# Performance work log

Measured on AMD Instinct MI355X. Metric: run time of the kernel, lower is better.

The kernel has to match this reference:

```python
import jax, jax.numpy as jnp
import numpy as np

SR = 44100.0
BLK = 512          # block_size (hop)
WL = 2048          # win_length
W4 = WL // 4
B, NF = 4, 512
L = NF * BLK


def _framewise_conv(src, kernels, pad_l, pad_r):
    """Per-(batch,frame) 1D cross-correlation via grouped conv.
    src: (B,F,blk), kernels: (B,F,kw) -> (B,F,blk+pad_l+pad_r-kw+1)."""
    b, f, blk = src.shape
    kw = kernels.shape[-1]
    s = jnp.pad(src, ((0, 0), (0, 0), (pad_l, pad_r))).reshape(1, b * f, blk + pad_l + pad_r)
    k = kernels.reshape(b * f, 1, kw)
    out = jax.lax.conv_general_dilated(
        s, k, window_strides=(1,), padding='VALID',
        feature_group_count=b * f, dimension_numbers=('NCH', 'OIH', 'NCH'))
    return out.reshape(b, f, -1)


def _overlap_add(frames, hop, out_len):
    """frames: (B,F,FL) -> (B,out_len) overlap-add with stride hop (== F.fold)."""
    b, f, fl = frames.shape
    idx = jnp.arange(f)[:, None] * hop + jnp.arange(fl)[None, :]  # (F,FL)
    out = jnp.zeros((b, out_len), frames.dtype)
    return out.at[:, idx].add(frames)


def setup_inputs() -> dict:
    key = jax.random.key(0)
    k1, k2, k3, k4, k5 = jax.random.split(key, 5)
    f0_frames = jax.random.uniform(k1, (B, NF, 1), jnp.float32) * 320.0 + 80.0  # 80-400 Hz
    hk = jax.random.normal(k2, (B, NF, WL), jnp.float32) * (1.0 / np.sqrt(WL))
    hks = jax.random.normal(k3, (B, NF, W4), jnp.float32) * (1.0 / np.sqrt(W4))
    nk = jax.random.normal(k4, (B, NF, W4), jnp.float32) * (1.0 / np.sqrt(W4))
    static_noise = jax.random.uniform(k5, (WL * 127,), jnp.float32) * 2.0 - 1.0
    return {"f0_frames": f0_frames, "harmonic_filt_kernel": hk,
            "harmonic_filt_kernel_short": hks, "noise_filt_kernel": nk,
            "static_noise": static_noise}


def reference(f0_frames, harmonic_filt_kernel, harmonic_filt_kernel_short,
              noise_filt_kernel, static_noise):
    b, nf, _ = f0_frames.shape
    # f0 upsampled to sample rate: (B, L)
    f0 = jnp.repeat(f0_frames, BLK, axis=2).reshape(b, -1)
    # phase accumulator, fractional part (f0 > 0 so frac == mod 1)
    x = jnp.mod(jnp.cumsum(f0 / SR, axis=1), 1.0)
    pix = jnp.pi * x
    a = jnp.round(SR / jnp.clip(f0, 20.0, None) * 0.5) * 2.0 + 1.0
    # band-limited impulse-train-like harmonic source (Dirichlet kernel)
    harmonic_source = jnp.where(pix < 1e-8, 1.0,
                                jnp.sin(a * pix) / (a * jnp.sin(pix)))
    harmonic_source = harmonic_source.reshape(b, nf, BLK)
    # tiled static noise, same for all batch items
    reps = L // static_noise.shape[0] + 1
    noise = jnp.tile(static_noise * 0.3162, reps)[:L].reshape(1, nf, BLK)
    noise = jnp.broadcast_to(noise, (b, nf, BLK))
    # short per-frame FIR on harmonic source and noise (kernel len WL//4)
    hs_short = _framewise_conv(harmonic_source, harmonic_filt_kernel_short, W4, W4 - 1)
    nz = _framewise_conv(noise, noise_filt_kernel, W4, W4 - 1)
    # overlap-add mix, crop to L samples
    mix = _overlap_add(nz + hs_short, BLK, L + W4)[:, :L]
    # long per-frame FIR (kernel len WL) on the mixed signal
    src2 = mix.reshape(b, nf, BLK)
    h2 = _framewise_conv(src2, harmonic_filt_kernel, WL, WL - 1)
    out = _overlap_add(h2, BLK, L + WL)[:, :L]
    return jnp.clip(out, -1.0, 1.0)
```

## Files before the change

kernel.cpp:

```cpp
#include <hip/hip_runtime.h>


#define BLKS  512
#define WL    2048
#define W4    512
#define NB    4
#define NFR   512
#define LTOT  (NFR*BLKS)
#define NCH   (LTOT/16)
#define SN_LEN 260096

typedef float f4 __attribute__((ext_vector_type(4)));

static __device__ __forceinline__ void seg4(const float* __restrict__ P, int c0,
                                            const float* __restrict__ S,
                                            float&a0,float&a1,float&a2,float&a3) {
    f4 A = *(const f4*)(P + c0 - 4);
    #pragma unroll 4
    for (int m0 = 0; m0 < 512; m0 += 4) {
        f4 B = *(const f4*)(P + c0 + m0);
        f4 x = *(const f4*)(S + m0);
        a0 += B.x*x.x; a0 += B.y*x.y; a0 += B.z*x.z; a0 += B.w*x.w;
        a1 += A.w*x.x; a1 += B.x*x.y; a1 += B.y*x.z; a1 += B.z*x.w;
        a2 += A.z*x.x; a2 += A.w*x.y; a2 += B.x*x.z; a2 += B.y*x.w;
        a3 += A.y*x.x; a3 += A.z*x.y; a3 += A.w*x.z; a3 += B.x*x.w;
        A = B;
    }
}

static __device__ __forceinline__ void segmix(const float* __restrict__ Ph,
                                              const float* __restrict__ Pn, int c0,
                                              const float* __restrict__ Sh,
                                              const float* __restrict__ Sn,
                                              float&a0,float&a1,float&a2,float&a3) {
    f4 Ah = *(const f4*)(Ph + c0 - 4);
    f4 An = *(const f4*)(Pn + c0 - 4);
    #pragma unroll 4
    for (int m0 = 0; m0 < 512; m0 += 4) {
        f4 Bh = *(const f4*)(Ph + c0 + m0);
        f4 Bn = *(const f4*)(Pn + c0 + m0);
        f4 xh = *(const f4*)(Sh + m0);
        f4 xr = *(const f4*)(Sn + m0);
        f4 xn; xn.x = xr.x*0.3162f; xn.y = xr.y*0.3162f;
               xn.z = xr.z*0.3162f; xn.w = xr.w*0.3162f;
        a0 += Bh.x*xh.x; a0 += Bn.x*xn.x;  a0 += Bh.y*xh.y; a0 += Bn.y*xn.y;
        a0 += Bh.z*xh.z; a0 += Bn.z*xn.z;  a0 += Bh.w*xh.w; a0 += Bn.w*xn.w;
        a1 += Ah.w*xh.x; a1 += An.w*xn.x;  a1 += Bh.x*xh.y; a1 += Bn.x*xn.y;
        a1 += Bh.y*xh.z; a1 += Bn.y*xn.z;  a1 += Bh.z*xh.w; a1 += Bn.z*xn.w;
        a2 += Ah.z*xh.x; a2 += An.z*xn.x;  a2 += Ah.w*xh.y; a2 += An.w*xn.y;
        a2 += Bh.x*xh.z; a2 += Bn.x*xn.z;  a2 += Bh.y*xh.w; a2 += Bn.y*xn.w;
        a3 += Ah.y*xh.x; a3 += An.y*xn.x;  a3 += Ah.z*xh.y; a3 += An.z*xn.y;
        a3 += Ah.w*xh.z; a3 += An.w*xn.z;  a3 += Bh.x*xh.w; a3 += Bn.x*xn.w;
        Ah = Bh; An = Bn;
    }
}

__global__ void __launch_bounds__(256) k_scan_a(const float* __restrict__ f0_frames,
                                                float* __restrict__ L0,
                                                float* __restrict__ L1) {
    int b = blockIdx.y;
    int chunk = blockIdx.x * 256 + threadIdx.x;
    int g0 = chunk * 16;
    float d = f0_frames[b*NFR + (g0 >> 9)] / 44100.0f;
    float* o = L0 + (size_t)b*LTOT + g0;
    float acc = 0.0f;
    #pragma unroll
    for (int j = 0; j < 16; ++j) { acc = acc + d; o[j] = acc; }
    L1[(size_t)b*NCH + chunk] = acc;
}

__global__ void __launch_bounds__(1024) k_scan_b(float* __restrict__ L1g) {
    __shared__ float sL2[1024];
    __shared__ float sL3[64];
    __shared__ float sL4[4];
    int b = blockIdx.x, tid = threadIdx.x;
    float* L1 = L1g + (size_t)b*NCH;
    {
        float* p = L1 + tid*16;
        float acc = 0.0f;
        #pragma unroll
        for (int j = 0; j < 16; ++j) { acc = acc + p[j]; p[j] = acc; }
        sL2[tid] = acc;
    }
    __syncthreads();
    if (tid < 64) {
        float acc = 0.0f;
        #pragma unroll
        for (int j = 0; j < 16; ++j) { acc = acc + sL2[tid*16+j]; sL2[tid*16+j] = acc; }
        sL3[tid] = acc;
    }
    __syncthreads();
    if (tid < 4) {
        float acc = 0.0f;
        #pragma unroll
        for (int j = 0; j < 16; ++j) { acc = acc + sL3[tid*16+j]; sL3[tid*16+j] = acc; }
        sL4[tid] = acc;
    }
    __syncthreads();
    if (tid == 0) {
        float acc = 0.0f;
        #pragma unroll
        for (int j = 0; j < 4; ++j) { acc = acc + sL4[j]; sL4[j] = acc; }
    }
    __syncthreads();
    if (tid >= 16 && tid < 64) sL3[tid] = sL3[tid] + sL4[tid/16 - 1];
    __syncthreads();
    if (tid >= 16) sL2[tid] = sL2[tid] + sL3[tid/16 - 1];
    __syncthreads();
    for (int i = tid; i < NCH; i += 1024)
        if (i >= 16) L1[i] = L1[i] + sL2[i/16 - 1];
}

__global__ void __launch_bounds__(256) k_source(const float* __restrict__ f0_frames,
                                                const float* __restrict__ L0,
                                                const float* __restrict__ L1,
                                                float* __restrict__ hs) {
    int F = blockIdx.x, b = blockIdx.y;
    int tid = threadIdx.x;
    float f0 = f0_frames[b*NFR + F];
    float af = rintf(44100.0f / fmaxf(f0, 20.0f) * 0.5f) * 2.0f + 1.0f;
    const float PIF = 3.14159274101257324f;
    for (int i = tid; i < BLKS; i += 256) {
        int g = F*BLKS + i;
        float c = L0[(size_t)b*LTOT + g];
        if (g >= 16) c = c + L1[(size_t)b*NCH + (g >> 4) - 1];
        float x = c - floorf(c);
        float pix = PIF * x;
        float v;
        if (pix < 1e-8f) v = 1.0f;
        else             v = sinf(af * pix) / (af * sinf(pix));
        hs[(size_t)b*LTOT + g] = v;
    }
}

__global__ void __launch_bounds__(128) k_mix(const float* __restrict__ hs,
                                             const float* __restrict__ sn,
                                             const float* __restrict__ hks,
                                             const float* __restrict__ nk,
                                             float* __restrict__ mixg) {
    __shared__ float Wh1[1024], Wn1[1024], Wh0[1024], Wn0[1024];
    int F = blockIdx.x, b = blockIdx.y, tid = threadIdx.x;
    const f4* khF4 = (const f4*)(hks + ((size_t)b*NFR + F)*W4);
    const f4* knF4 = (const f4*)(nk  + ((size_t)b*NFR + F)*W4);
    f4 z; z.x = z.y = z.z = z.w = 0.0f;
    for (int i = tid; i < 256; i += 128) {
        ((f4*)Wh1)[i] = (i < 128) ? khF4[i] : z;
        ((f4*)Wn1)[i] = (i < 128) ? knF4[i] : z;
        ((f4*)Wh0)[i] = (i >= 128 && F >= 1) ? khF4[i - 256] : z;
        ((f4*)Wn0)[i] = (i >= 128 && F >= 1) ? knF4[i - 256] : z;
    }
    __syncthreads();
    int j0 = tid * 4;
    float a0=0,a1=0,a2=0,a3=0;
    const float* hsF = hs + (size_t)b*LTOT + (size_t)F*BLKS;
    segmix(Wh1, Wn1, 512 - j0, hsF, sn + (F*BLKS) % SN_LEN, a0,a1,a2,a3);
    if (F >= 1)
        segmix(Wh0, Wn0, 512 - j0, hsF - BLKS, sn + ((F-1)*BLKS) % SN_LEN,
               a0,a1,a2,a3);
    f4 r; r.x=a0; r.y=a1; r.z=a2; r.w=a3;
    *(f4*)(mixg + (size_t)b*LTOT + (size_t)F*BLKS + j0) = r;
}

__global__ void __launch_bounds__(128) k_out(const float* __restrict__ mixg,
                                             const float* __restrict__ hk,
                                             float* __restrict__ outp) {
    __shared__ float Wc[5][1024];
    int F = blockIdx.x, b = blockIdx.y, tid = threadIdx.x;
    f4 z; z.x = z.y = z.z = z.w = 0.0f;
    #pragma unroll
    for (int q = 0; q < 5; ++q) {
        int fs = F - 4 + q;
        const f4* row4 = (const f4*)(hk + ((size_t)b*NFR + fs)*WL);
        f4* Wp = (f4*)Wc[q];
        for (int i = tid; i < 256; i += 128) {
            f4 v = z;
            if (fs >= 0) {
                if (q == 0)      { if (i >= 128) v = row4[i - 128]; }
                else if (q == 4) { if (i < 128)  v = row4[384 + i]; }
                else             v = row4[128*(q-1) + i];
            }
            Wp[i] = v;
        }
    }
    __syncthreads();
    int j0 = tid * 4;
    float a0=0,a1=0,a2=0,a3=0;
    const float* mb = mixg + (size_t)b*LTOT;
    #pragma unroll 1
    for (int q = 1; q <= 3; ++q) {
        int fs = F - 4 + q;
        if (fs < 0) continue;
        seg4(Wc[q], 512 - j0, mb + (size_t)fs*BLKS, a0,a1,a2,a3);
    }
    seg4(Wc[4], 512 - j0, mb + (size_t)F*BLKS, a0,a1,a2,a3);
    if (F >= 4)
        seg4(Wc[0], 512 - j0, mb + (size_t)(F-4)*BLKS, a0,a1,a2,a3);
    f4 r;
    r.x = fminf(fmaxf(a0, -1.0f), 1.0f);
    r.y = fminf(fmaxf(a1, -1.0f), 1.0f);
    r.z = fminf(fmaxf(a2, -1.0f), 1.0f);
    r.w = fminf(fmaxf(a3, -1.0f), 1.0f);
    *(f4*)(outp + (size_t)b*LTOT + (size_t)F*BLKS + j0) = r;
}

extern "C" void kernel_launch(void* const* d_in, const int* in_sizes, int n_in,
                              void* d_out, int out_size, void* d_ws, size_t ws_size,
                              hipStream_t stream) {
    const float* f0  = (const float*)d_in[0];
    const float* hk  = (const float*)d_in[1];
    const float* hks = (const float*)d_in[2];
    const float* nk  = (const float*)d_in[3];
    const float* sn  = (const float*)d_in[4];
    float* outp = (float*)d_out;

    float* ws   = (float*)d_ws;
    float* L0   = ws;
    float* L1   = L0 + (size_t)NB*LTOT;
    float* hsb  = L1 + (size_t)NB*NCH;
    float* mixg = hsb + (size_t)NB*LTOT;

    hipLaunchKernelGGL(k_scan_a, dim3(64, NB),  dim3(256),  0, stream, f0, L0, L1);
    hipLaunchKernelGGL(k_scan_b, dim3(NB),      dim3(1024), 0, stream, L1);
    hipLaunchKernelGGL(k_source, dim3(NFR, NB), dim3(256),  0, stream, f0, L0, L1, hsb);
    hipLaunchKernelGGL(k_mix,    dim3(NFR, NB), dim3(128),  0, stream, hsb, sn, hks, nk, mixg);
    hipLaunchKernelGGL(k_out,    dim3(NFR, NB), dim3(128),  0, stream, mixg, hk, outp);
}
```

Baseline: 171.9 us.

## Compute eight outputs per thread in k_out with swizzled LDS kernel layout

The long-FIR k_out kernel now runs 64 threads per block, each producing 8 consecutive outputs instead of 4. Each LDS kernel load and each signal load is therefore reused across twice as many accumulators, which cuts LDS and global traffic per FMA. The kernel window is stored in LDS with an XOR swizzle on the f4 index to avoid bank conflicts from the new 8-float per-thread stride. In exchange, per-block parallelism halves (64-thread blocks, one wave) and register pressure rises.

```diff
diff --git a/kernel.cpp b/kernel.cpp
--- a/kernel.cpp
+++ b/kernel.cpp
@@ -12,19 +12,30 @@
 
 typedef float f4 __attribute__((ext_vector_type(4)));
 
-static __device__ __forceinline__ void seg4(const float* __restrict__ P, int c0,
-                                            const float* __restrict__ S,
-                                            float&a0,float&a1,float&a2,float&a3) {
-    f4 A = *(const f4*)(P + c0 - 4);
+static __device__ __forceinline__ f4 ldswz(const float* __restrict__ W, int fi) {
+    int w = fi >> 2;
+    return ((const f4*)W)[w ^ ((w >> 3) & 1)];
+}
+
+static __device__ __forceinline__ void seg8s(const float* __restrict__ W, int c0,
+                                             const float* __restrict__ S,
+                                             float&a0,float&a1,float&a2,float&a3,
+                                             float&a4,float&a5,float&a6,float&a7) {
+    f4 A = ldswz(W, c0 - 8);
+    f4 B = ldswz(W, c0 - 4);
     #pragma unroll 4
     for (int m0 = 0; m0 < 512; m0 += 4) {
-        f4 B = *(const f4*)(P + c0 + m0);
+        f4 C = ldswz(W, c0 + m0);
         f4 x = *(const f4*)(S + m0);
-        a0 += B.x*x.x; a0 += B.y*x.y; a0 += B.z*x.z; a0 += B.w*x.w;
-        a1 += A.w*x.x; a1 += B.x*x.y; a1 += B.y*x.z; a1 += B.z*x.w;
-        a2 += A.z*x.x; a2 += A.w*x.y; a2 += B.x*x.z; a2 += B.y*x.w;
-        a3 += A.y*x.x; a3 += A.z*x.y; a3 += A.w*x.z; a3 += B.x*x.w;
-        A = B;
+        a0 += C.x*x.x; a0 += C.y*x.y; a0 += C.z*x.z; a0 += C.w*x.w;
+        a1 += B.w*x.x; a1 += C.x*x.y; a1 += C.y*x.z; a1 += C.z*x.w;
+        a2 += B.z*x.x; a2 += B.w*x.y; a2 += C.x*x.z; a2 += C.y*x.w;
+        a3 += B.y*x.x; a3 += B.z*x.y; a3 += B.w*x.z; a3 += C.x*x.w;
+        a4 += B.x*x.x; a4 += B.y*x.y; a4 += B.z*x.z; a4 += B.w*x.w;
+        a5 += A.w*x.x; a5 += B.x*x.y; a5 += B.y*x.z; a5 += B.z*x.w;
+        a6 += A.z*x.x; a6 += A.w*x.y; a6 += B.x*x.z; a6 += B.y*x.w;
+        a7 += A.y*x.x; a7 += A.z*x.y; a7 += A.w*x.z; a7 += B.x*x.w;
+        A = B; B = C;
     }
 }
 
@@ -161,9 +172,9 @@
     *(f4*)(mixg + (size_t)b*LTOT + (size_t)F*BLKS + j0) = r;
 }
 
-__global__ void __launch_bounds__(128) k_out(const float* __restrict__ mixg,
-                                             const float* __restrict__ hk,
-                                             float* __restrict__ outp) {
+__global__ void __launch_bounds__(64) k_out(const float* __restrict__ mixg,
+                                            const float* __restrict__ hk,
+                                            float* __restrict__ outp) {
     __shared__ float Wc[5][1024];
     int F = blockIdx.x, b = blockIdx.y, tid = threadIdx.x;
     f4 z; z.x = z.y = z.z = z.w = 0.0f;
@@ -172,35 +183,43 @@
         int fs = F - 4 + q;
         const f4* row4 = (const f4*)(hk + ((size_t)b*NFR + fs)*WL);
         f4* Wp = (f4*)Wc[q];
-        for (int i = tid; i < 256; i += 128) {
+        #pragma unroll
+        for (int k = 0; k < 4; ++k) {
+            int w = tid + 64*k;
             f4 v = z;
             if (fs >= 0) {
-                if (q == 0)      { if (i >= 128) v = row4[i - 128]; }
-                else if (q == 4) { if (i < 128)  v = row4[384 + i]; }
-                else             v = row4[128*(q-1) + i];
+                if (q == 0)      { if (w >= 128) v = row4[w - 128]; }
+                else if (q == 4) { if (w < 128)  v = row4[384 + w]; }
+                else             v = row4[128*(q-1) + w];
             }
-            Wp[i] = v;
+            Wp[w ^ ((w >> 3) & 1)] = v;
         }
     }
     __syncthreads();
-    int j0 = tid * 4;
-    float a0=0,a1=0,a2=0,a3=0;
+    int j0 = tid * 8;
+    int c0 = 512 - j0;
+    float a0=0,a1=0,a2=0,a3=0,a4=0,a5=0,a6=0,a7=0;
     const float* mb = mixg + (size_t)b*LTOT;
     #pragma unroll 1
     for (int q = 1; q <= 3; ++q) {
         int fs = F - 4 + q;
         if (fs < 0) continue;
-        seg4(Wc[q], 512 - j0, mb + (size_t)fs*BLKS, a0,a1,a2,a3);
-    }
-    seg4(Wc[4], 512 - j0, mb + (size_t)F*BLKS, a0,a1,a2,a3);
+        seg8s(Wc[q], c0, mb + (size_t)fs*BLKS, a0,a1,a2,a3,a4,a5,a6,a7);
+    }
+    seg8s(Wc[4], c0, mb + (size_t)F*BLKS, a0,a1,a2,a3,a4,a5,a6,a7);
     if (F >= 4)
-        seg4(Wc[0], 512 - j0, mb + (size_t)(F-4)*BLKS, a0,a1,a2,a3);
-    f4 r;
-    r.x = fminf(fmaxf(a0, -1.0f), 1.0f);
-    r.y = fminf(fmaxf(a1, -1.0f), 1.0f);
-    r.z = fminf(fmaxf(a2, -1.0f), 1.0f);
-    r.w = fminf(fmaxf(a3, -1.0f), 1.0f);
-    *(f4*)(outp + (size_t)b*LTOT + (size_t)F*BLKS + j0) = r;
+        seg8s(Wc[0], c0, mb + (size_t)(F-4)*BLKS, a0,a1,a2,a3,a4,a5,a6,a7);
+    float* o = outp + (size_t)b*LTOT + (size_t)F*BLKS + j0;
+    f4 r0, r1;
+    r0.x = fminf(fmaxf(a0, -1.0f), 1.0f);
+    r0.y = fminf(fmaxf(a1, -1.0f), 1.0f);
+    r0.z = fminf(fmaxf(a2, -1.0f), 1.0f);
+    r0.w = fminf(fmaxf(a3, -1.0f), 1.0f);
+    r1.x = fminf(fmaxf(a4, -1.0f), 1.0f);
+    r1.y = fminf(fmaxf(a5, -1.0f), 1.0f);
+    r1.z = fminf(fmaxf(a6, -1.0f), 1.0f);
+    r1.w = fminf(fmaxf(a7, -1.0f), 1.0f);
+    *(f4*)o = r0; *(f4*)(o + 4) = r1;
 }
 
 extern "C" void kernel_launch(void* const* d_in, const int* in_sizes, int n_in,
@@ -223,5 +242,5 @@
     hipLaunchKernelGGL(k_scan_b, dim3(NB),      dim3(1024), 0, stream, L1);
     hipLaunchKernelGGL(k_source, dim3(NFR, NB), dim3(256),  0, stream, f0, L0, L1, hsb);
     hipLaunchKernelGGL(k_mix,    dim3(NFR, NB), dim3(128),  0, stream, hsb, sn, hks, nk, mixg);
-    hipLaunchKernelGGL(k_out,    dim3(NFR, NB), dim3(128),  0, stream, mixg, hk, outp);
-}
+    hipLaunchKernelGGL(k_out,    dim3(NFR, NB), dim3(64),   0, stream, mixg, hk, outp);
+}
```

After: 181.6 us. 1.06x slower.
